# Kernel tuning notes

Measured on AMD Instinct MI355X. Metric: run time of the kernel, lower is better.

## Reference

```python
import jax, jax.numpy as jnp
import numpy as np

H, Q, D, V = 256, 64, 512, 34
L, N, T = 1024, 64, 256


def _mlp(x, W0, b0, W1, b1):
    # two-layer MLP with ELU on hidden (matches MLP with nn.ELU activation)
    return jax.nn.elu(x @ W0.T + b0) @ W1.T + b1


def _lstm_cell(x, h, c, Wih, Whh, bih, bhh):
    gates = x @ Wih.T + bih + h @ Whh.T + bhh
    i, f, g, o = jnp.split(gates, 4, axis=-1)  # PyTorch LSTMCell gate order
    i, f, o = jax.nn.sigmoid(i), jax.nn.sigmoid(f), jax.nn.sigmoid(o)
    c_new = f * c + i * jnp.tanh(g)
    h_new = o * jnp.tanh(c_new)
    return h_new, c_new


def _attn(q, key, value, mask):
    # q: [N,Q], key: [N,L,Q], value: [N,L,H], mask: [N,L]
    scores = jnp.einsum('nlq,nq->nl', key, q)
    a = jax.nn.softmax(scores, axis=-1) * mask
    a = a / jnp.sum(a, axis=-1, keepdims=True)
    return jnp.einsum('nl,nlh->nh', a, value)


def setup_inputs() -> dict:
    key = jax.random.key(0)
    ks = iter(jax.random.split(key, 64))

    def rn(shape, s=0.05):
        return jax.random.normal(next(ks), shape, jnp.float32) * s

    inp = {
        'seqs': rn((L, N, D), 1.0),
        'seq_lens': jax.random.randint(next(ks), (N,), L // 2, L + 1),
        'labels': jax.random.randint(next(ks), (T, N), 0, V),
        'emb': rn((V, H)),
        'inith': rn((3, H)),
        'initc': rn((3, H)),
    }
    in_sizes = [2 * H, H, H]
    for i in range(3):
        inp[f'Wih{i}'] = rn((4 * H, in_sizes[i]))
        inp[f'Whh{i}'] = rn((4 * H, H))
        inp[f'bih{i}'] = rn((4 * H,))
        inp[f'bhh{i}'] = rn((4 * H,))
    inp['qW0'] = rn((H, H)); inp['qb0'] = rn((H,))
    inp['qW1'] = rn((Q, H)); inp['qb1'] = rn((Q,))
    inp['kW0'] = rn((D, D)); inp['kb0'] = rn((D,))
    inp['kW1'] = rn((Q, D)); inp['kb1'] = rn((Q,))
    inp['vW0'] = rn((H, D)); inp['vb0'] = rn((H,))
    inp['vW1'] = rn((H, H)); inp['vb1'] = rn((H,))
    inp['outW'] = rn((V, 2 * H)); inp['outb'] = rn((V,))
    return inp


def reference(seqs, seq_lens, labels, emb, inith, initc,
              Wih0, Whh0, bih0, bhh0, Wih1, Whh1, bih1, bhh1,
              Wih2, Whh2, bih2, bhh2,
              qW0, qb0, qW1, qb1, kW0, kb0, kW1, kb1,
              vW0, vb0, vW1, vb1, outW, outb):
    T_, N_ = labels.shape
    L_ = seqs.shape[0]
    lstm = [(Wih0, Whh0, bih0, bhh0), (Wih1, Whh1, bih1, bhh1), (Wih2, Whh2, bih2, bhh2)]

    char_input = emb[labels]                                   # [T,N,H]
    key = _mlp(seqs, kW0, kb0, kW1, kb1).transpose(1, 0, 2)    # [N,L,Q]
    value = _mlp(seqs, vW0, vb0, vW1, vb1).transpose(1, 0, 2)  # [N,L,H]
    mask = (jnp.arange(L_)[None, :] < seq_lens[:, None]).astype(seqs.dtype)

    h = jnp.tile(inith[:, None, :], (1, N_, 1))  # [3,N,H]
    c = jnp.tile(initc[:, None, :], (1, N_, 1))
    q = _mlp(h[2], qW0, qb0, qW1, qb1)
    prev_ctx = _attn(q, key, value, mask)

    def step(carry, x_t):
        h, c, ctx = carry
        xin = jnp.concatenate([ctx, x_t], axis=1)  # [N,2H]
        hs, cs = [], []
        for i in range(3):
            nh, nc = _lstm_cell(xin, h[i], c[i], *lstm[i])
            hs.append(nh); cs.append(nc)
            xin = nh
        h = jnp.stack(hs); c = jnp.stack(cs)
        q = _mlp(h[2], qW0, qb0, qW1, qb1)
        ctx = _attn(q, key, value, mask)
        out = jnp.concatenate([ctx, h[2]], axis=1) @ outW.T + outb  # [N,V]
        return (h, c, ctx), out

    _, outs = jax.lax.scan(step, (h, c, prev_ctx), char_input)
    return outs  # [T,N,V]
```

## Files before the change

kernel.cpp:

```cpp
#include <hip/hip_runtime.h>
#include <cstddef>

#define DEV static __device__ __forceinline__
typedef unsigned long long ull;

DEV float b2f(unsigned short u){ unsigned int i=((unsigned int)u)<<16; float f; __builtin_memcpy(&f,&i,4); return f; }
DEV float lo16(unsigned int u){ unsigned int i=u<<16; float f; __builtin_memcpy(&f,&i,4); return f; }
DEV float hi16(unsigned int u){ unsigned int i=u&0xffff0000u; float f; __builtin_memcpy(&f,&i,4); return f; }
DEV unsigned short f2b(float f){ unsigned int i; __builtin_memcpy(&i,&f,4); unsigned int r=(i+0x7fffu+((i>>16)&1u))>>16; return (unsigned short)r; }
DEV float sigf(float x){ return 1.f/(1.f+__expf(-x)); }
DEV float eluf(float x){ return x>0.f ? x : (__expf(x)-1.f); }
DEV float gload(const void* p, long i, int f32){
  return f32 ? ((const float*)p)[i] : b2f(((const unsigned short*)p)[i]);
}
DEV ull pk(float f, unsigned tag){ unsigned b; __builtin_memcpy(&b,&f,4); return ((ull)tag<<32)|b; }
DEV float upk(ull u){ unsigned b=(unsigned)u; float f; __builtin_memcpy(&f,&b,4); return f; }
DEV void ast64(ull* p, ull v){ __hip_atomic_store(p, v, __ATOMIC_RELAXED, __HIP_MEMORY_SCOPE_AGENT); }
DEV ull ald64(const ull* p){ return __hip_atomic_load(p, __ATOMIC_RELAXED, __HIP_MEMORY_SCOPE_AGENT); }

__global__ __launch_bounds__(64) void sniff(const void* __restrict__ seqs,
                                            const void* __restrict__ seq_lens,
                                            int* __restrict__ flags)
{
  __shared__ int cnt;
  if (threadIdx.x==0) cnt=0;
  __syncthreads();
  const unsigned short* u = (const unsigned short*)seqs;
  int sane=0;
  for (int i=threadIdx.x;i<1024;i+=64){
    int e = (u[i]>>7)&0xFF;
    if (e>=0x70 && e<=0x8F) sane++;
  }
  atomicAdd(&cnt, sane);
  __syncthreads();
  if (threadIdx.x==0){
    flags[0] = (cnt < 820) ? 1 : 0;
    const int* s = (const int*)seq_lens;
    flags[1] = ((s[1]|s[3]|s[5]|s[7])==0) ? 1 : 0;
  }
}

__global__ __launch_bounds__(256) void prep_transpose(
    const void* __restrict__ Wih0, const void* __restrict__ Whh0,
    const void* __restrict__ Wih1, const void* __restrict__ Whh1,
    const void* __restrict__ Wih2, const void* __restrict__ Whh2,
    const void* __restrict__ kW0,  const void* __restrict__ kW1,
    const void* __restrict__ vW0,  const void* __restrict__ vW1,
    const void* __restrict__ qW0,  const void* __restrict__ qW1,
    const void* __restrict__ bih0, const void* __restrict__ bhh0,
    const void* __restrict__ bih1, const void* __restrict__ bhh1,
    const void* __restrict__ bih2, const void* __restrict__ bhh2,
    const void* __restrict__ outW, const void* __restrict__ inith,
    const void* __restrict__ initc, const void* __restrict__ qb0,
    const void* __restrict__ qb1,  const void* __restrict__ outb,
    const int* __restrict__ flags,
    unsigned short* __restrict__ Wl0, unsigned short* __restrict__ Wl1,
    unsigned short* __restrict__ Wl2,
    unsigned short* __restrict__ kW0T, unsigned short* __restrict__ kW1T,
    unsigned short* __restrict__ vW0T, unsigned short* __restrict__ vW1T,
    unsigned short* __restrict__ qW0T, unsigned short* __restrict__ qW1T,
    float* __restrict__ bsum,
    unsigned short* __restrict__ outWc, unsigned short* __restrict__ inithc,
    unsigned short* __restrict__ initcc, unsigned short* __restrict__ qb0c,
    unsigned short* __restrict__ qb1c,  unsigned short* __restrict__ outbc)
{
  const int f32 = flags[0];
  int idx = blockIdx.x*256 + threadIdx.x;
  if (idx < 524288){ int r=idx&131071, k=r>>8, gi=r&255;
    int g = ((gi>>6)<<8) + ((idx>>17)<<6) + (gi&63);
    Wl0[idx] = f2b((k<256)? gload(Wih0,(long)g*512+k,f32) : gload(Whh0,(long)g*256+(k-256),f32)); return; }
  idx -= 524288;
  if (idx < 524288){ int r=idx&131071, k=r>>8, gi=r&255;
    int g = ((gi>>6)<<8) + ((idx>>17)<<6) + (gi&63);
    Wl1[idx] = f2b((k<256)? gload(Wih1,(long)g*256+k,f32) : gload(Whh1,(long)g*256+(k-256),f32)); return; }
  idx -= 524288;
  if (idx < 524288){ int r=idx&131071, k=r>>8, gi=r&255;
    int g = ((gi>>6)<<8) + ((idx>>17)<<6) + (gi&63);
    Wl2[idx] = f2b((k<256)? gload(Wih2,(long)g*256+k,f32) : gload(Whh2,(long)g*256+(k-256),f32)); return; }
  idx -= 524288;
  if (idx < 262144){ int k=idx>>9, j=idx&511; kW0T[idx]=f2b(gload(kW0,(long)j*512+k,f32)); return; }
  idx -= 262144;
  if (idx < 32768){ int k=idx>>6, j=idx&63; kW1T[idx]=f2b(gload(kW1,(long)j*512+k,f32)); return; }
  idx -= 32768;
  if (idx < 131072){ int k=idx>>8, j=idx&255; vW0T[idx]=f2b(gload(vW0,(long)j*512+k,f32)); return; }
  idx -= 131072;
  if (idx < 65536){ int k=idx>>8, j=idx&255; vW1T[idx]=f2b(gload(vW1,(long)j*256+k,f32)); return; }
  idx -= 65536;
  if (idx < 65536){ int k=idx>>8, j=idx&255; qW0T[idx]=f2b(gload(qW0,(long)j*256+k,f32)); return; }
  idx -= 65536;
  if (idx < 16384){ int k=idx>>6, j=idx&63; qW1T[idx]=f2b(gload(qW1,(long)j*256+k,f32)); return; }
  idx -= 16384;
  if (idx < 3072){ int l=idx>>10, r=idx&1023, pp=r>>8, gi=r&255;
    int g = ((gi>>6)<<8) + (pp<<6) + (gi&63);
    const void* bi = (l==0)?bih0:((l==1)?bih1:bih2);
    const void* bh = (l==0)?bhh0:((l==1)?bhh1:bhh2);
    bsum[idx] = gload(bi,g,f32)+gload(bh,g,f32); return; }
  idx -= 3072;
  if (idx < 17408){ outWc[idx]=f2b(gload(outW,idx,f32)); return; }
  idx -= 17408;
  if (idx < 768){ inithc[idx]=f2b(gload(inith,idx,f32)); return; }
  idx -= 768;
  if (idx < 768){ initcc[idx]=f2b(gload(initc,idx,f32)); return; }
  idx -= 768;
  if (idx < 256){ qb0c[idx]=f2b(gload(qb0,idx,f32)); return; }
  idx -= 256;
  if (idx < 64){ qb1c[idx]=f2b(gload(qb1,idx,f32)); return; }
  idx -= 64;
  if (idx < 34){ outbc[idx]=f2b(gload(outb,idx,f32)); return; }
}

__global__ __launch_bounds__(256) void prep_ge(
    const void* __restrict__ emb,
    const void* __restrict__ Wih0,
    const int* __restrict__ flags,
    float* __restrict__ gep)
{
  __shared__ float ev[256];
  const int f32 = flags[0];
  const int v = blockIdx.x, tid = threadIdx.x;
  ev[tid] = gload(emb,(long)v*256+tid,f32);
  __syncthreads();
  #pragma unroll
  for (int j=0;j<4;j++){
    const int g = tid*4+j;
    float a = 0.f;
    #pragma unroll 4
    for (int k=0;k<256;k++) a += ev[k]*gload(Wih0,(long)g*512+256+k,f32);
    int pp = (g>>6)&3, gi = ((g>>8)<<6)|(g&63);
    gep[((size_t)pp*34+v)*256+gi] = a;
  }
}

__global__ __launch_bounds__(256) void key_mlp(
    const void* __restrict__ seqs,
    const unsigned short* __restrict__ kW0T, const void* __restrict__ kb0,
    const unsigned short* __restrict__ kW1T, const void* __restrict__ kb1,
    const int* __restrict__ flags,
    unsigned short* __restrict__ keyT)
{
  __shared__ float Xt[16*512];
  __shared__ unsigned short Hd[16*512];
  const int f32 = flags[0];
  const int tid = threadIdx.x;
  const int R0 = blockIdx.x*16;
  for (int i=tid;i<8192;i+=256) Xt[i] = gload(seqs,(long)R0*512+i,f32);
  __syncthreads();
  {
    const int j0 = 2*tid;
    float acc0[16], acc1[16];
    #pragma unroll
    for (int r=0;r<16;r++){ acc0[r]=0.f; acc1[r]=0.f; }
    for (int k=0;k<512;k++){
      ushort2 w = *reinterpret_cast<const ushort2*>(kW0T + (size_t)k*512 + j0);
      float w0=b2f(w.x), w1=b2f(w.y);
      #pragma unroll
      for (int r=0;r<16;r++){ float x = Xt[r*512+k]; acc0[r]+=x*w0; acc1[r]+=x*w1; }
    }
    float b0v=gload(kb0,j0,f32), b1v=gload(kb0,j0+1,f32);
    #pragma unroll
    for (int r=0;r<16;r++){
      Hd[r*512+j0]   = f2b(eluf(acc0[r]+b0v));
      Hd[r*512+j0+1] = f2b(eluf(acc1[r]+b1v));
    }
  }
  __syncthreads();
  {
    const int j = tid & 63;
    const int rbase = tid >> 6;
    float acc[4] = {0.f,0.f,0.f,0.f};
    for (int k=0;k<512;k++){
      float w = b2f(kW1T[(size_t)k*64 + j]);
      #pragma unroll
      for (int m=0;m<4;m++) acc[m] += b2f(Hd[(rbase+4*m)*512 + k]) * w;
    }
    float bv = gload(kb1,j,f32);
    #pragma unroll
    for (int m=0;m<4;m++){
      int R = R0 + rbase + 4*m;
      int l = R >> 6, n = R & 63;
      keyT[((size_t)(n*64 + j))*1024 + l] = f2b(acc[m]+bv);
    }
  }
}

__global__ __launch_bounds__(256) void value_mlp(
    const void* __restrict__ seqs,
    const unsigned short* __restrict__ vW0T, const void* __restrict__ vb0,
    const unsigned short* __restrict__ vW1T, const void* __restrict__ vb1,
    const int* __restrict__ flags,
    unsigned short* __restrict__ value)
{
  __shared__ float Xt[16*512];
  __shared__ float Hd[16*256];
  const int f32 = flags[0];
  const int tid = threadIdx.x;
  const int R0 = blockIdx.x*16;
  for (int i=tid;i<8192;i+=256) Xt[i] = gload(seqs,(long)R0*512+i,f32);
  __syncthreads();
  {
    const int j0 = 2*(tid & 127);
    const int rh = tid >> 7;
    float acc0[8], acc1[8];
    #pragma unroll
    for (int r=0;r<8;r++){ acc0[r]=0.f; acc1[r]=0.f; }
    for (int k=0;k<512;k++){
      ushort2 w = *reinterpret_cast<const ushort2*>(vW0T + (size_t)k*256 + j0);
      float w0=b2f(w.x), w1=b2f(w.y);
      #pragma unroll
      for (int r=0;r<8;r++){ float x = Xt[(rh*8+r)*512+k]; acc0[r]+=x*w0; acc1[r]+=x*w1; }
    }
    float b0v=gload(vb0,j0,f32), b1v=gload(vb0,j0+1,f32);
    #pragma unroll
    for (int r=0;r<8;r++){
      Hd[(rh*8+r)*256+j0]   = eluf(acc0[r]+b0v);
      Hd[(rh*8+r)*256+j0+1] = eluf(acc1[r]+b1v);
    }
  }
  __syncthreads();
  {
    const int j = tid;
    float acc[16];
    #pragma unroll
    for (int r=0;r<16;r++) acc[r]=0.f;
    for (int k=0;k<256;k++){
      float w = b2f(vW1T[(size_t)k*256 + j]);
      #pragma unroll
      for (int r=0;r<16;r++) acc[r] += Hd[r*256+k]*w;
    }
    float bv = gload(vb1,j,f32);
    #pragma unroll
    for (int r=0;r<16;r++){
      int R = R0 + r; int l = R>>6, n = R&63;
      value[((size_t)n*1024 + l)*256 + j] = f2b(acc[r]+bv);
    }
  }
}

__global__ __launch_bounds__(256) void zero_hbuf(ull* __restrict__ f){
  int i = blockIdx.x*256 + threadIdx.x;
  if (i < 115200) f[i] = 0;
}

__global__ __launch_bounds__(512, 1) void speller(
    const unsigned short* __restrict__ keyT,
    const unsigned short* __restrict__ value,
    const unsigned short* __restrict__ Wl0,
    const unsigned short* __restrict__ Wl1,
    const unsigned short* __restrict__ Wl2,
    const unsigned short* __restrict__ qW0T,
    const unsigned short* __restrict__ qW1T,
    const float* __restrict__ bsum_p,
    const float* __restrict__ gep,
    const unsigned short* __restrict__ inithc,
    const unsigned short* __restrict__ initcc,
    const unsigned short* __restrict__ qb0c,
    const unsigned short* __restrict__ qb1c,
    const unsigned short* __restrict__ outWc,
    const unsigned short* __restrict__ outbc,
    const int* __restrict__ labels,
    const int* __restrict__ seq_lens,
    const int* __restrict__ dflags,
    ull* __restrict__ hbw,
    void* __restrict__ out)
{
  extern __shared__ char smem_dyn[];
  unsigned short* vlds = (unsigned short*)smem_dyn;

  __shared__ float sacc[4096];
  __shared__ float inc[512];
  __shared__ float garr[256];
  __shared__ float h0[256], h1[256], h2[256], ctx[256];
  __shared__ float cloc[3][64];
  __shared__ float hsl[3][64];
  __shared__ float xq[256];
  __shared__ float qv[64];
  __shared__ float sarr[256], earr[256];
  __shared__ float red[128];
  __shared__ float wf[4];
  __shared__ float pcl[256];
  __shared__ float statl[8];

  const int tid = threadIdx.x;
  const int n = blockIdx.x >> 2;
  const int p = blockIdx.x & 3;
  const int f32o = dflags[0];
  const int i64 = dflags[1];
  const int slen = i64 ? seq_lens[2*n] : seq_lens[n];

  ull* mb   = hbw + (size_t)n*1800;
  ull* H0w  = mb;
  ull* H1w  = mb + 256;
  ull* H2w  = mb + 512;
  ull* PCw  = mb + 768;
  ull* STw  = mb + 1792;

  {
    const uint4* src = (const uint4*)(value + ((size_t)n*1024 + p*256)*256);
    uint4* dst = (uint4*)vlds;
    for (int i=tid;i<16384;i+=512) dst[i] = src[i];
  }
  if (tid < 256){ h0[tid]=b2f(inithc[tid]); h1[tid]=b2f(inithc[256+tid]); h2[tid]=b2f(inithc[512+tid]); }
  if (tid < 64){
    cloc[0][tid]=b2f(initcc[p*64+tid]);
    cloc[1][tid]=b2f(initcc[256+p*64+tid]);
    cloc[2][tid]=b2f(initcc[512+p*64+tid]);
  }
  __syncthreads();

  auto lstm = [&](const unsigned short* W, const float* bs, const float* ger,
                  int layer, ull* Hw, unsigned tag){
    const int go8 = tid & 31, ks = tid >> 5;
    const unsigned short* wp = W + (size_t)p*131072 + (size_t)ks*32*256 + go8*8;
    const float* xin = inc + ks*32;
    float a0=0.f,a1=0.f,a2=0.f,a3=0.f,a4=0.f,a5=0.f,a6=0.f,a7=0.f;
    #pragma unroll 16
    for (int k=0;k<32;k++){
      float x = xin[k];
      uint4 w = *reinterpret_cast<const uint4*>(wp + (size_t)k*256);
      a0 += x*lo16(w.x); a1 += x*hi16(w.x);
      a2 += x*lo16(w.y); a3 += x*hi16(w.y);
      a4 += x*lo16(w.z); a5 += x*hi16(w.z);
      a6 += x*lo16(w.w); a7 += x*hi16(w.w);
    }
    float* sb = sacc + ks*256 + go8*8;
    sb[0]=a0; sb[1]=a1; sb[2]=a2; sb[3]=a3; sb[4]=a4; sb[5]=a5; sb[6]=a6; sb[7]=a7;
    __syncthreads();
    if (tid < 256){
      float s = bs[tid] + (ger ? ger[tid] : 0.f);
      #pragma unroll
      for (int u=0;u<16;u++) s += sacc[u*256+tid];
      garr[tid] = s;
    }
    __syncthreads();
    if (tid < 64){
      float gi=garr[tid], gf=garr[64+tid], gg=garr[128+tid], go=garr[192+tid];
      float cc = sigf(gf)*cloc[layer][tid] + sigf(gi)*tanhf(gg);
      float hh = sigf(go)*tanhf(cc);
      cloc[layer][tid]=cc;
      hsl[layer][tid]=hh;
      ast64(Hw + p*64 + tid, pk(hh, tag));
    }
  };

  auto gather_h = [&](const ull* Hw, int layer, unsigned tag, float* hdst){
    __syncthreads();
    if (tid < 256){
      int sp = tid >> 6; float v;
      if (sp == p) v = hsl[layer][tid & 63];
      else { const ull* w = Hw + tid; ull u = ald64(w);
             while ((unsigned)(u>>32) != tag) u = ald64(w);
             v = upk(u); }
      hdst[tid] = v;
    }
    __syncthreads();
  };

  auto attn = [&](unsigned tag){
    {
      const int j = tid & 255, kh = tid >> 8;
      const unsigned short* qp = qW0T + (size_t)(kh*128)*256 + j;
      float a = 0.f;
      #pragma unroll 8
      for (int k=0;k<128;k++) a += h2[kh*128+k]*b2f(qp[(size_t)k*256]);
      sacc[kh*256 + j] = a;
    }
    __syncthreads();
    if (tid < 256) xq[tid] = eluf(sacc[tid]+sacc[256+tid] + b2f(qb0c[tid]));
    __syncthreads();
    {
      const int qc = tid & 63, k8 = tid >> 6;
      float a = 0.f;
      const unsigned short* qp = qW1T + qc;
      #pragma unroll 8
      for (int k=0;k<32;k++){ int kk = k8*32+k; a += xq[kk]*b2f(qp[(size_t)kk*64]); }
      sacc[k8*64+qc] = a;
    }
    __syncthreads();
    if (tid < 64){
      float s=0.f;
      #pragma unroll
      for (int u=0;u<8;u++) s += sacc[u*64+tid];
      qv[tid] = s + b2f(qb1c[tid]);
    }
    __syncthreads();
    {
      const int lp = tid & 127, qh = tid >> 7;
      float a0=0.f,a1=0.f;
      const unsigned short* kp = keyT + (size_t)n*65536 + (size_t)qh*16*1024 + p*256 + 2*lp;
      #pragma unroll 8
      for (int q=0;q<16;q++){
        ushort2 w = *reinterpret_cast<const ushort2*>(kp + (size_t)q*1024);
        float qq = qv[qh*16+q];
        a0 += qq*b2f(w.x); a1 += qq*b2f(w.y);
      }
      sacc[qh*256+2*lp]=a0; sacc[qh*256+2*lp+1]=a1;
    }
    __syncthreads();
    if (tid < 256){
      float s = sacc[tid]+sacc[256+tid]+sacc[512+tid]+sacc[768+tid];
      sarr[tid] = (p*256+tid < slen) ? s : -1e30f;
    }
    __syncthreads();
    if (tid < 128) red[tid] = fmaxf(sarr[tid], sarr[tid+128]);
    __syncthreads();
    for (int s=64;s>0;s>>=1){ if (tid<s) red[tid]=fmaxf(red[tid],red[tid+s]); __syncthreads(); }
    const float pmax = red[0];
    __syncthreads();
    if (tid < 256) earr[tid] = (p*256+tid < slen) ? __expf(sarr[tid]-pmax) : 0.f;
    __syncthreads();
    if (tid < 128) red[tid] = earr[tid]+earr[tid+128];
    __syncthreads();
    for (int s=64;s>0;s>>=1){ if (tid<s) red[tid]+=red[tid+s]; __syncthreads(); }
    const float psum = red[0];
    {
      const int hp = tid & 127, lq = tid >> 7;
      float a0=0.f,a1=0.f;
      const unsigned short* vp = vlds + (size_t)(lq*64)*256 + 2*hp;
      #pragma unroll 8
      for (int l=0;l<64;l++){
        ushort2 w = *reinterpret_cast<const ushort2*>(vp + (size_t)l*256);
        float e = earr[lq*64+l];
        a0 += e*b2f(w.x); a1 += e*b2f(w.y);
      }
      sacc[lq*256+2*hp]=a0; sacc[lq*256+2*hp+1]=a1;
    }
    __syncthreads();
    if (tid < 256){
      float v = sacc[tid]+sacc[256+tid]+sacc[512+tid]+sacc[768+tid];
      pcl[tid] = v;
      ast64(PCw + p*256 + tid, pk(v, tag));
    }
    if (tid == 0){ ast64(STw + p*2, pk(pmax, tag)); ast64(STw + p*2 + 1, pk(psum, tag)); }
    if (tid < 8){
      int q = tid >> 1, ix = tid & 1; float v;
      if (q == p) v = ix ? psum : pmax;
      else { const ull* w = STw + q*2 + ix; ull u = ald64(w);
             while ((unsigned)(u>>32) != tag) u = ald64(w);
             v = upk(u); }
      statl[tid] = v;
    }
    __syncthreads();
    if (tid == 0){
      float m0=statl[0], s0=statl[1], m1=statl[2], s1=statl[3];
      float m2=statl[4], s2=statl[5], m3=statl[6], s3=statl[7];
      float M = fmaxf(fmaxf(m0,m1),fmaxf(m2,m3));
      float w0=__expf(m0-M), w1=__expf(m1-M), w2=__expf(m2-M), w3=__expf(m3-M);
      float inv = 1.f/(s0*w0+s1*w1+s2*w2+s3*w3);
      wf[0]=w0*inv; wf[1]=w1*inv; wf[2]=w2*inv; wf[3]=w3*inv;
    }
    __syncthreads();
    if (tid < 256){
      float acc = pcl[tid]*wf[p];
      #pragma unroll
      for (int q=0;q<4;q++){
        if (q == p) continue;
        const ull* w = PCw + q*256 + tid; ull u = ald64(w);
        while ((unsigned)(u>>32) != tag) u = ald64(w);
        acc += upk(u)*wf[q];
      }
      ctx[tid] = acc;
    }
    __syncthreads();
  };

  attn(1);

  for (int t=0;t<256;t++){
    const unsigned tb = 4*(unsigned)t;
    const int lab = i64 ? labels[2*(t*64+n)] : labels[t*64+n];
    if (tid < 256){ inc[tid]=ctx[tid]; inc[256+tid]=h0[tid]; }
    __syncthreads();
    lstm(Wl0, bsum_p + p*256, gep + ((size_t)p*34+lab)*256, 0, H0w, tb+2);
    gather_h(H0w, 0, tb+2, h0);
    if (tid < 256){ inc[tid]=h0[tid]; inc[256+tid]=h1[tid]; }
    __syncthreads();
    lstm(Wl1, bsum_p + 1024 + p*256, nullptr, 1, H1w, tb+3);
    gather_h(H1w, 1, tb+3, h1);
    if (tid < 256){ inc[tid]=h1[tid]; inc[256+tid]=h2[tid]; }
    __syncthreads();
    lstm(Wl2, bsum_p + 2048 + p*256, nullptr, 2, H2w, tb+4);
    gather_h(H2w, 2, tb+4, h2);
    attn(tb+5);
    {
      const int ri = tid >> 6, kk = tid & 63;
      const int r = 4*ri + p;
      float acc = 0.f;
      const unsigned short* wr = outWc + (size_t)r*512 + kk;
      #pragma unroll
      for (int s=0;s<4;s++) acc += ctx[s*64+kk]*b2f(wr[s*64]);
      #pragma unroll
      for (int s=0;s<4;s++) acc += h2[s*64+kk]*b2f(wr[256+s*64]);
      #pragma unroll
      for (int off=32; off>0; off>>=1) acc += __shfl_down(acc, off);
      if (kk==0){
        float v = acc + b2f(outbc[r]);
        size_t oi = ((size_t)(t*64+n))*34 + r;
        if (f32o) ((float*)out)[oi]=v; else ((unsigned short*)out)[oi]=f2b(v);
      }
      if (p < 2 && tid < 64){
        const int r2 = 32+p;
        float a2=0.f;
        const unsigned short* wr2 = outWc + (size_t)r2*512 + tid;
        #pragma unroll
        for (int s=0;s<4;s++) a2 += ctx[s*64+tid]*b2f(wr2[s*64]);
        #pragma unroll
        for (int s=0;s<4;s++) a2 += h2[s*64+tid]*b2f(wr2[256+s*64]);
        #pragma unroll
        for (int off=32; off>0; off>>=1) a2 += __shfl_down(a2, off);
        if (tid==0){
          float v = a2 + b2f(outbc[r2]);
          size_t oi = ((size_t)(t*64+n))*34 + r2;
          if (f32o) ((float*)out)[oi]=v; else ((unsigned short*)out)[oi]=f2b(v);
        }
      }
    }
  }
}

extern "C" void kernel_launch(void* const* d_in, const int* in_sizes, int n_in,
                              void* d_out, int out_size, void* d_ws, size_t ws_size,
                              hipStream_t stream) {
  const void* seqs  = d_in[0];
  const int* seq_lens = (const int*)d_in[1];
  const int* labels   = (const int*)d_in[2];
  const void* emb   = d_in[3];
  const void* inith = d_in[4];
  const void* initc = d_in[5];
  const void* Wih0 = d_in[6];  const void* Whh0 = d_in[7];
  const void* bih0 = d_in[8];  const void* bhh0 = d_in[9];
  const void* Wih1 = d_in[10]; const void* Whh1 = d_in[11];
  const void* bih1 = d_in[12]; const void* bhh1 = d_in[13];
  const void* Wih2 = d_in[14]; const void* Whh2 = d_in[15];
  const void* bih2 = d_in[16]; const void* bhh2 = d_in[17];
  const void* qW0 = d_in[18];  const void* qb0 = d_in[19];
  const void* qW1 = d_in[20];  const void* qb1 = d_in[21];
  const void* kW0 = d_in[22];  const void* kb0 = d_in[23];
  const void* kW1 = d_in[24];  const void* kb1 = d_in[25];
  const void* vW0 = d_in[26];  const void* vb0 = d_in[27];
  const void* vW1 = d_in[28];  const void* vb1 = d_in[29];
  const void* outW = d_in[30]; const void* outb = d_in[31];

  char* ws = (char*)d_ws;
  unsigned short* keyT  = (unsigned short*)(ws);
  unsigned short* value = (unsigned short*)(ws + 8388608);
  unsigned short* Wl0   = (unsigned short*)(ws + 41943040);
  unsigned short* Wl1   = (unsigned short*)(ws + 42991616);
  unsigned short* Wl2   = (unsigned short*)(ws + 44040192);
  unsigned short* kW0T  = (unsigned short*)(ws + 45088768);
  unsigned short* kW1T  = (unsigned short*)(ws + 45613056);
  unsigned short* vW0T  = (unsigned short*)(ws + 45678592);
  unsigned short* vW1T  = (unsigned short*)(ws + 45940736);
  unsigned short* qW0T  = (unsigned short*)(ws + 46071808);
  unsigned short* qW1T  = (unsigned short*)(ws + 46202880);
  float*          bsum  = (float*)(ws + 46235648);
  float*          gep   = (float*)(ws + 46247936);
  unsigned short* outWc = (unsigned short*)(ws + 46387200);
  unsigned short* inithc= (unsigned short*)(ws + 46422016);
  unsigned short* initcc= (unsigned short*)(ws + 46423552);
  unsigned short* qb0c  = (unsigned short*)(ws + 46425088);
  unsigned short* qb1c  = (unsigned short*)(ws + 46425600);
  unsigned short* outbc = (unsigned short*)(ws + 46425728);
  int*            dflags= (int*)(ws + 46425856);
  ull* hbw = (ull*)(ws + 45088768);

  sniff<<<dim3(1), dim3(64), 0, stream>>>(seqs, seq_lens, dflags);
  prep_transpose<<<dim3(8472), dim3(256), 0, stream>>>(
      Wih0,Whh0,Wih1,Whh1,Wih2,Whh2, kW0,kW1,vW0,vW1,qW0,qW1,
      bih0,bhh0,bih1,bhh1,bih2,bhh2,
      outW,inith,initc,qb0,qb1,outb, dflags,
      Wl0,Wl1,Wl2,kW0T,kW1T,vW0T,vW1T,qW0T,qW1T,bsum,
      outWc,inithc,initcc,qb0c,qb1c,outbc);
  prep_ge<<<dim3(34), dim3(256), 0, stream>>>(emb, Wih0, dflags, gep);
  key_mlp<<<dim3(4096), dim3(256), 0, stream>>>(seqs, kW0T, kb0, kW1T, kb1, dflags, keyT);
  value_mlp<<<dim3(4096), dim3(256), 0, stream>>>(seqs, vW0T, vb0, vW1T, vb1, dflags, value);
  zero_hbuf<<<dim3(450), dim3(256), 0, stream>>>(hbw);
  hipFuncSetAttribute((const void*)speller, hipFuncAttributeMaxDynamicSharedMemorySize, 131072);
  speller<<<dim3(256), dim3(512), 131072, stream>>>(
      keyT, value, Wl0, Wl1, Wl2, qW0T, qW1T, bsum, gep,
      inithc, initcc, qb0c, qb1c, outWc, outbc, labels, seq_lens, dflags,
      hbw, d_out);
}
```

Measured before the change: 8.248 ms.

## Co-locate cooperating blocks per XCD and use L2-scoped flag exchange

Remaps block indices so the four blocks that cooperate on one sequence are likely to land on the same XCD. Each block reads its XCC id from a hardware register and publishes it, and when all four match, h, context and softmax statistics are exchanged through sc0 stores and loads that stay in the shared L2 instead of going device-wide. Tags now carry a per-launch salt so stale mailbox entries cannot match. The tree reductions for the softmax max and sum are replaced with wavefront shuffles. The cost is reliance on undocumented scheduling behaviour and memory-scope semantics, plus dual posting (atomic and sc0 store) on every write.

```diff
diff --git a/kernel.cpp b/kernel.cpp
--- a/kernel.cpp
+++ b/kernel.cpp
@@ -17,6 +17,15 @@
 DEV float upk(ull u){ unsigned b=(unsigned)u; float f; __builtin_memcpy(&f,&b,4); return f; }
 DEV void ast64(ull* p, ull v){ __hip_atomic_store(p, v, __ATOMIC_RELAXED, __HIP_MEMORY_SCOPE_AGENT); }
 DEV ull ald64(const ull* p){ return __hip_atomic_load(p, __ATOMIC_RELAXED, __HIP_MEMORY_SCOPE_AGENT); }
+DEV void st_sc0(ull* p, ull v){
+  asm volatile("global_store_dwordx2 %0, %1, off sc0" :: "v"(p), "v"(v) : "memory");
+}
+DEV ull ld_sc0(const ull* p){
+  ull r;
+  asm volatile("global_load_dwordx2 %0, %1, off sc0\n\ts_waitcnt vmcnt(0)"
+               : "=v"(r) : "v"(p) : "memory");
+  return r;
+}
 
 __global__ __launch_bounds__(64) void sniff(const void* __restrict__ seqs,
                                             const void* __restrict__ seq_lens,
@@ -238,7 +247,7 @@
 
 __global__ __launch_bounds__(256) void zero_hbuf(ull* __restrict__ f){
   int i = blockIdx.x*256 + threadIdx.x;
-  if (i < 115200) f[i] = 0;
+  if (i < 115456) ast64(&f[i], 0);
 }
 
 __global__ __launch_bounds__(512, 1) void speller(
@@ -274,25 +283,37 @@
   __shared__ float hsl[3][64];
   __shared__ float xq[256];
   __shared__ float qv[64];
-  __shared__ float sarr[256], earr[256];
-  __shared__ float red[128];
+  __shared__ float earr[256];
+  __shared__ float red[16];
   __shared__ float wf[4];
   __shared__ float pcl[256];
   __shared__ float statl[8];
+  __shared__ int   xcls[4];
 
   const int tid = threadIdx.x;
-  const int n = blockIdx.x >> 2;
-  const int p = blockIdx.x & 3;
+  const int bx  = (int)blockIdx.x;
+  const int slot = bx >> 3;
+  const int n = ((slot >> 2) << 3) | (bx & 7);
+  const int p = slot & 3;
   const int f32o = dflags[0];
   const int i64 = dflags[1];
   const int slen = i64 ? seq_lens[2*n] : seq_lens[n];
 
-  ull* mb   = hbw + (size_t)n*1800;
+  ull* mb   = hbw + (size_t)n*1804;
   ull* H0w  = mb;
   ull* H1w  = mb + 256;
   ull* H2w  = mb + 512;
   ull* PCw  = mb + 768;
   ull* STw  = mb + 1792;
+  ull* XCw  = mb + 1800;
+
+  int myxcc;
+  asm volatile("s_getreg_b32 %0, hwreg(20, 0, 32)" : "=s"(myxcc));
+  myxcc &= 0xf;
+  if (tid == 0){
+    unsigned salt = (unsigned)(__builtin_amdgcn_s_memrealtime() >> 4) & 0x1fffffu;
+    ast64(XCw + p, ((ull)1u<<32) | (unsigned)myxcc | (salt<<4));
+  }
 
   {
     const uint4* src = (const uint4*)(value + ((size_t)n*1024 + p*256)*256);
@@ -306,6 +327,37 @@
     cloc[2][tid]=b2f(initcc[512+p*64+tid]);
   }
   __syncthreads();
+
+  if (tid < 4){
+    const ull* w = XCw + tid; ull u = ald64(w);
+    while ((unsigned)(u>>32) != 1u) u = ald64(w);
+    xcls[tid] = (int)(unsigned)u;
+  }
+  __syncthreads();
+  const unsigned xl0=(unsigned)xcls[0], xl1=(unsigned)xcls[1],
+                 xl2=(unsigned)xcls[2], xl3=(unsigned)xcls[3];
+  const bool fastmb = (((xl0^xl1)|(xl1^xl2)|(xl2^xl3)) & 0xfu) == 0u;
+  const unsigned tagbase = (xl0 >> 4) << 11;
+
+  auto post = [&](ull* w, ull v){
+    ast64(w, v);
+    if (fastmb) st_sc0(w, v);
+  };
+  auto pollw = [&](const ull* w, unsigned tag)->float{
+    ull u;
+    if (fastmb){
+      u = ld_sc0(w);
+      int spins = 0;
+      while ((unsigned)(u>>32) != tag){
+        ++spins;
+        u = (spins < 128 || (spins & 1)) ? ld_sc0(w) : ald64(w);
+      }
+    } else {
+      u = ald64(w);
+      while ((unsigned)(u>>32) != tag) u = ald64(w);
+    }
+    return upk(u);
+  };
 
   auto lstm = [&](const unsigned short* W, const float* bs, const float* ger,
                   int layer, ull* Hw, unsigned tag){
@@ -338,7 +390,7 @@
       float hh = sigf(go)*tanhf(cc);
       cloc[layer][tid]=cc;
       hsl[layer][tid]=hh;
-      ast64(Hw + p*64 + tid, pk(hh, tag));
+      post(Hw + p*64 + tid, pk(hh, tag));
     }
   };
 
@@ -347,9 +399,7 @@
     if (tid < 256){
       int sp = tid >> 6; float v;
       if (sp == p) v = hsl[layer][tid & 63];
-      else { const ull* w = Hw + tid; ull u = ald64(w);
-             while ((unsigned)(u>>32) != tag) u = ald64(w);
-             v = upk(u); }
+      else v = pollw(Hw + tid, tag);
       hdst[tid] = v;
     }
     __syncthreads();
@@ -396,22 +446,31 @@
       sacc[qh*256+2*lp]=a0; sacc[qh*256+2*lp+1]=a1;
     }
     __syncthreads();
-    if (tid < 256){
-      float s = sacc[tid]+sacc[256+tid]+sacc[512+tid]+sacc[768+tid];
-      sarr[tid] = (p*256+tid < slen) ? s : -1e30f;
-    }
-    __syncthreads();
-    if (tid < 128) red[tid] = fmaxf(sarr[tid], sarr[tid+128]);
-    __syncthreads();
-    for (int s=64;s>0;s>>=1){ if (tid<s) red[tid]=fmaxf(red[tid],red[tid+s]); __syncthreads(); }
-    const float pmax = red[0];
-    __syncthreads();
-    if (tid < 256) earr[tid] = (p*256+tid < slen) ? __expf(sarr[tid]-pmax) : 0.f;
-    __syncthreads();
-    if (tid < 128) red[tid] = earr[tid]+earr[tid+128];
-    __syncthreads();
-    for (int s=64;s>0;s>>=1){ if (tid<s) red[tid]+=red[tid+s]; __syncthreads(); }
-    const float psum = red[0];
+    float pmax, psum;
+    {
+      float s = -1e30f;
+      if (tid < 256){
+        s = sacc[tid]+sacc[256+tid]+sacc[512+tid]+sacc[768+tid];
+        if (p*256+tid >= slen) s = -1e30f;
+      }
+      float m = s;
+      #pragma unroll
+      for (int off=32; off; off>>=1) m = fmaxf(m, __shfl_xor(m, off));
+      if ((tid&63)==0) red[tid>>6] = m;
+      __syncthreads();
+      pmax = fmaxf(fmaxf(red[0],red[1]),fmaxf(red[2],red[3]));
+      float e = 0.f;
+      if (tid < 256){
+        e = (p*256+tid < slen) ? __expf(s - pmax) : 0.f;
+        earr[tid] = e;
+      }
+      float ss = e;
+      #pragma unroll
+      for (int off=32; off; off>>=1) ss += __shfl_xor(ss, off);
+      if ((tid&63)==0) red[8+(tid>>6)] = ss;
+      __syncthreads();
+      psum = red[8]+red[9]+red[10]+red[11];
+    }
     {
       const int hp = tid & 127, lq = tid >> 7;
       float a0=0.f,a1=0.f;
@@ -428,15 +487,13 @@
     if (tid < 256){
       float v = sacc[tid]+sacc[256+tid]+sacc[512+tid]+sacc[768+tid];
       pcl[tid] = v;
-      ast64(PCw + p*256 + tid, pk(v, tag));
-    }
-    if (tid == 0){ ast64(STw + p*2, pk(pmax, tag)); ast64(STw + p*2 + 1, pk(psum, tag)); }
+      post(PCw + p*256 + tid, pk(v, tag));
+    }
+    if (tid == 0){ post(STw + p*2, pk(pmax, tag)); post(STw + p*2 + 1, pk(psum, tag)); }
     if (tid < 8){
       int q = tid >> 1, ix = tid & 1; float v;
       if (q == p) v = ix ? psum : pmax;
-      else { const ull* w = STw + q*2 + ix; ull u = ald64(w);
-             while ((unsigned)(u>>32) != tag) u = ald64(w);
-             v = upk(u); }
+      else v = pollw(STw + q*2 + ix, tag);
       statl[tid] = v;
     }
     __syncthreads();
@@ -454,19 +511,17 @@
       #pragma unroll
       for (int q=0;q<4;q++){
         if (q == p) continue;
-        const ull* w = PCw + q*256 + tid; ull u = ald64(w);
-        while ((unsigned)(u>>32) != tag) u = ald64(w);
-        acc += upk(u)*wf[q];
+        acc += pollw(PCw + q*256 + tid, tag)*wf[q];
       }
       ctx[tid] = acc;
     }
     __syncthreads();
   };
 
-  attn(1);
+  attn(tagbase+1);
 
   for (int t=0;t<256;t++){
-    const unsigned tb = 4*(unsigned)t;
+    const unsigned tb = tagbase + 4*(unsigned)t;
     const int lab = i64 ? labels[2*(t*64+n)] : labels[t*64+n];
     if (tid < 256){ inc[tid]=ctx[tid]; inc[256+tid]=h0[tid]; }
     __syncthreads();
@@ -573,7 +628,7 @@
   prep_ge<<<dim3(34), dim3(256), 0, stream>>>(emb, Wih0, dflags, gep);
   key_mlp<<<dim3(4096), dim3(256), 0, stream>>>(seqs, kW0T, kb0, kW1T, kb1, dflags, keyT);
   value_mlp<<<dim3(4096), dim3(256), 0, stream>>>(seqs, vW0T, vb0, vW1T, vb1, dflags, value);
-  zero_hbuf<<<dim3(450), dim3(256), 0, stream>>>(hbw);
+  zero_hbuf<<<dim3(451), dim3(256), 0, stream>>>(hbw);
   hipFuncSetAttribute((const void*)speller, hipFuncAttributeMaxDynamicSharedMemorySize, 131072);
   speller<<<dim3(256), dim3(512), 131072, stream>>>(
       keyT, value, Wl0, Wl1, Wl2, qW0T, qW1T, bsum, gep,
```

After: 21.70 ms. +163.1%, slower.

## Cut barriers in speller step: fused input staging, wave-shuffle softmax, vectorized q-MLP weights

Applied to the files above, without the earlier changes.

Each recurrent step of the persistent speller kernel loses several __syncthreads: the LSTM input staging moves into gather_h and the attention tail, and the softmax max/sum tree reductions become wave-level shuffle reductions. The q-MLP weights are re-laid out in prep so each thread reads 8 bf16 values per 128-bit load instead of scalar strided loads. The cross-block context spin-wait now issues all three polls before looping. The goal is a shorter serial critical path per timestep, at the cost of a more complex weight layout and more coupling between the step phases.

```diff
diff --git a/kernel.cpp b/kernel.cpp
--- a/kernel.cpp
+++ b/kernel.cpp
@@ -58,7 +58,7 @@
     unsigned short* __restrict__ Wl2,
     unsigned short* __restrict__ kW0T, unsigned short* __restrict__ kW1T,
     unsigned short* __restrict__ vW0T, unsigned short* __restrict__ vW1T,
-    unsigned short* __restrict__ qW0T, unsigned short* __restrict__ qW1T,
+    unsigned short* __restrict__ qW0v, unsigned short* __restrict__ qW1v,
     float* __restrict__ bsum,
     unsigned short* __restrict__ outWc, unsigned short* __restrict__ inithc,
     unsigned short* __restrict__ initcc, unsigned short* __restrict__ qb0c,
@@ -86,9 +86,13 @@
   idx -= 131072;
   if (idx < 65536){ int k=idx>>8, j=idx&255; vW1T[idx]=f2b(gload(vW1,(long)j*256+k,f32)); return; }
   idx -= 65536;
-  if (idx < 65536){ int k=idx>>8, j=idx&255; qW0T[idx]=f2b(gload(qW0,(long)j*256+k,f32)); return; }
+  if (idx < 65536){
+    int k8=idx>>11, j=(idx>>3)&255, kk=idx&7; int k=k8*8+kk;
+    qW0v[idx]=f2b(gload(qW0,(long)j*256+k,f32)); return; }
   idx -= 65536;
-  if (idx < 16384){ int k=idx>>6, j=idx&63; qW1T[idx]=f2b(gload(qW1,(long)j*256+k,f32)); return; }
+  if (idx < 16384){
+    int k8=idx>>11, qc=(idx>>5)&63, kk=idx&31; int k=k8*32+kk;
+    qW1v[idx]=f2b(gload(qW1,(long)qc*256+k,f32)); return; }
   idx -= 16384;
   if (idx < 3072){ int l=idx>>10, r=idx&1023, pp=r>>8, gi=r&255;
     int g = ((gi>>6)<<8) + (pp<<6) + (gi&63);
@@ -247,8 +251,8 @@
     const unsigned short* __restrict__ Wl0,
     const unsigned short* __restrict__ Wl1,
     const unsigned short* __restrict__ Wl2,
-    const unsigned short* __restrict__ qW0T,
-    const unsigned short* __restrict__ qW1T,
+    const unsigned short* __restrict__ qW0v,
+    const unsigned short* __restrict__ qW1v,
     const float* __restrict__ bsum_p,
     const float* __restrict__ gep,
     const unsigned short* __restrict__ inithc,
@@ -274,8 +278,8 @@
   __shared__ float hsl[3][64];
   __shared__ float xq[256];
   __shared__ float qv[64];
-  __shared__ float sarr[256], earr[256];
-  __shared__ float red[128];
+  __shared__ float earr[256];
+  __shared__ float red[16];
   __shared__ float wf[4];
   __shared__ float pcl[256];
   __shared__ float statl[8];
@@ -342,7 +346,8 @@
     }
   };
 
-  auto gather_h = [&](const ull* Hw, int layer, unsigned tag, float* hdst){
+  auto gather_h = [&](const ull* Hw, int layer, unsigned tag, float* hdst,
+                      const float* nexth){
     __syncthreads();
     if (tid < 256){
       int sp = tid >> 6; float v;
@@ -351,6 +356,7 @@
              while ((unsigned)(u>>32) != tag) u = ald64(w);
              v = upk(u); }
       hdst[tid] = v;
+      if (nexth){ inc[tid] = v; inc[256+tid] = nexth[tid]; }
     }
     __syncthreads();
   };
@@ -358,10 +364,17 @@
   auto attn = [&](unsigned tag){
     {
       const int j = tid & 255, kh = tid >> 8;
-      const unsigned short* qp = qW0T + (size_t)(kh*128)*256 + j;
+      const uint4* qp = (const uint4*)qW0v + (size_t)(kh*16)*256 + j;
       float a = 0.f;
-      #pragma unroll 8
-      for (int k=0;k<128;k++) a += h2[kh*128+k]*b2f(qp[(size_t)k*256]);
+      #pragma unroll
+      for (int k8=0;k8<16;k8++){
+        uint4 w = qp[(size_t)k8*256];
+        const float* hb = h2 + kh*128 + k8*8;
+        a += hb[0]*lo16(w.x)+hb[1]*hi16(w.x)
+           + hb[2]*lo16(w.y)+hb[3]*hi16(w.y)
+           + hb[4]*lo16(w.z)+hb[5]*hi16(w.z)
+           + hb[6]*lo16(w.w)+hb[7]*hi16(w.w);
+      }
       sacc[kh*256 + j] = a;
     }
     __syncthreads();
@@ -369,10 +382,17 @@
     __syncthreads();
     {
       const int qc = tid & 63, k8 = tid >> 6;
+      const uint4* qp = (const uint4*)qW1v + (size_t)(k8*64+qc)*4;
       float a = 0.f;
-      const unsigned short* qp = qW1T + qc;
-      #pragma unroll 8
-      for (int k=0;k<32;k++){ int kk = k8*32+k; a += xq[kk]*b2f(qp[(size_t)kk*64]); }
+      #pragma unroll
+      for (int u=0;u<4;u++){
+        uint4 w = qp[u];
+        const float* xb = xq + k8*32 + u*8;
+        a += xb[0]*lo16(w.x)+xb[1]*hi16(w.x)
+           + xb[2]*lo16(w.y)+xb[3]*hi16(w.y)
+           + xb[4]*lo16(w.z)+xb[5]*hi16(w.z)
+           + xb[6]*lo16(w.w)+xb[7]*hi16(w.w);
+      }
       sacc[k8*64+qc] = a;
     }
     __syncthreads();
@@ -396,22 +416,31 @@
       sacc[qh*256+2*lp]=a0; sacc[qh*256+2*lp+1]=a1;
     }
     __syncthreads();
-    if (tid < 256){
-      float s = sacc[tid]+sacc[256+tid]+sacc[512+tid]+sacc[768+tid];
-      sarr[tid] = (p*256+tid < slen) ? s : -1e30f;
-    }
-    __syncthreads();
-    if (tid < 128) red[tid] = fmaxf(sarr[tid], sarr[tid+128]);
-    __syncthreads();
-    for (int s=64;s>0;s>>=1){ if (tid<s) red[tid]=fmaxf(red[tid],red[tid+s]); __syncthreads(); }
-    const float pmax = red[0];
-    __syncthreads();
-    if (tid < 256) earr[tid] = (p*256+tid < slen) ? __expf(sarr[tid]-pmax) : 0.f;
-    __syncthreads();
-    if (tid < 128) red[tid] = earr[tid]+earr[tid+128];
-    __syncthreads();
-    for (int s=64;s>0;s>>=1){ if (tid<s) red[tid]+=red[tid+s]; __syncthreads(); }
-    const float psum = red[0];
+    float pmax, psum;
+    {
+      float s = -1e30f;
+      if (tid < 256){
+        s = sacc[tid]+sacc[256+tid]+sacc[512+tid]+sacc[768+tid];
+        if (p*256+tid >= slen) s = -1e30f;
+      }
+      float m = s;
+      #pragma unroll
+      for (int off=32; off; off>>=1) m = fmaxf(m, __shfl_xor(m, off));
+      if ((tid&63)==0) red[tid>>6] = m;
+      __syncthreads();
+      pmax = fmaxf(fmaxf(red[0],red[1]),fmaxf(red[2],red[3]));
+      float e = 0.f;
+      if (tid < 256){
+        e = (p*256+tid < slen) ? __expf(s - pmax) : 0.f;
+        earr[tid] = e;
+      }
+      float ss = e;
+      #pragma unroll
+      for (int off=32; off; off>>=1) ss += __shfl_xor(ss, off);
+      if ((tid&63)==0) red[8+(tid>>6)] = ss;
+      __syncthreads();
+      psum = red[8]+red[9]+red[10]+red[11];
+    }
     {
       const int hp = tid & 127, lq = tid >> 7;
       float a0=0.f,a1=0.f;
@@ -450,15 +479,18 @@
     }
     __syncthreads();
     if (tid < 256){
-      float acc = pcl[tid]*wf[p];
-      #pragma unroll
-      for (int q=0;q<4;q++){
-        if (q == p) continue;
-        const ull* w = PCw + q*256 + tid; ull u = ald64(w);
-        while ((unsigned)(u>>32) != tag) u = ald64(w);
-        acc += upk(u)*wf[q];
-      }
+      const int q0=(p+1)&3, q1=(p+2)&3, q2=(p+3)&3;
+      const ull* w0 = PCw + q0*256 + tid;
+      const ull* w1 = PCw + q1*256 + tid;
+      const ull* w2 = PCw + q2*256 + tid;
+      ull u0=ald64(w0), u1=ald64(w1), u2=ald64(w2);
+      while ((unsigned)(u0>>32) != tag) u0 = ald64(w0);
+      while ((unsigned)(u1>>32) != tag) u1 = ald64(w1);
+      while ((unsigned)(u2>>32) != tag) u2 = ald64(w2);
+      float acc = pcl[tid]*wf[p] + upk(u0)*wf[q0] + upk(u1)*wf[q1] + upk(u2)*wf[q2];
       ctx[tid] = acc;
+      inc[tid] = acc;
+      inc[256+tid] = h0[tid];
     }
     __syncthreads();
   };
@@ -468,18 +500,12 @@
   for (int t=0;t<256;t++){
     const unsigned tb = 4*(unsigned)t;
     const int lab = i64 ? labels[2*(t*64+n)] : labels[t*64+n];
-    if (tid < 256){ inc[tid]=ctx[tid]; inc[256+tid]=h0[tid]; }
-    __syncthreads();
     lstm(Wl0, bsum_p + p*256, gep + ((size_t)p*34+lab)*256, 0, H0w, tb+2);
-    gather_h(H0w, 0, tb+2, h0);
-    if (tid < 256){ inc[tid]=h0[tid]; inc[256+tid]=h1[tid]; }
-    __syncthreads();
+    gather_h(H0w, 0, tb+2, h0, h1);
     lstm(Wl1, bsum_p + 1024 + p*256, nullptr, 1, H1w, tb+3);
-    gather_h(H1w, 1, tb+3, h1);
-    if (tid < 256){ inc[tid]=h1[tid]; inc[256+tid]=h2[tid]; }
-    __syncthreads();
+    gather_h(H1w, 1, tb+3, h1, h2);
     lstm(Wl2, bsum_p + 2048 + p*256, nullptr, 2, H2w, tb+4);
-    gather_h(H2w, 2, tb+4, h2);
+    gather_h(H2w, 2, tb+4, h2, nullptr);
     attn(tb+5);
     {
       const int ri = tid >> 6, kk = tid & 63;
@@ -550,8 +576,8 @@
   unsigned short* kW1T  = (unsigned short*)(ws + 45613056);
   unsigned short* vW0T  = (unsigned short*)(ws + 45678592);
   unsigned short* vW1T  = (unsigned short*)(ws + 45940736);
-  unsigned short* qW0T  = (unsigned short*)(ws + 46071808);
-  unsigned short* qW1T  = (unsigned short*)(ws + 46202880);
+  unsigned short* qW0v  = (unsigned short*)(ws + 46071808);
+  unsigned short* qW1v  = (unsigned short*)(ws + 46202880);
   float*          bsum  = (float*)(ws + 46235648);
   float*          gep   = (float*)(ws + 46247936);
   unsigned short* outWc = (unsigned short*)(ws + 46387200);
@@ -568,7 +594,7 @@
       Wih0,Whh0,Wih1,Whh1,Wih2,Whh2, kW0,kW1,vW0,vW1,qW0,qW1,
       bih0,bhh0,bih1,bhh1,bih2,bhh2,
       outW,inith,initc,qb0,qb1,outb, dflags,
-      Wl0,Wl1,Wl2,kW0T,kW1T,vW0T,vW1T,qW0T,qW1T,bsum,
+      Wl0,Wl1,Wl2,kW0T,kW1T,vW0T,vW1T,qW0v,qW1v,bsum,
       outWc,inithc,initcc,qb0c,qb1c,outbc);
   prep_ge<<<dim3(34), dim3(256), 0, stream>>>(emb, Wih0, dflags, gep);
   key_mlp<<<dim3(4096), dim3(256), 0, stream>>>(seqs, kW0T, kb0, kW1T, kb1, dflags, keyT);
@@ -576,7 +602,7 @@
   zero_hbuf<<<dim3(450), dim3(256), 0, stream>>>(hbw);
   hipFuncSetAttribute((const void*)speller, hipFuncAttributeMaxDynamicSharedMemorySize, 131072);
   speller<<<dim3(256), dim3(512), 131072, stream>>>(
-      keyT, value, Wl0, Wl1, Wl2, qW0T, qW1T, bsum, gep,
+      keyT, value, Wl0, Wl1, Wl2, qW0v, qW1v, bsum, gep,
       inithc, initcc, qb0c, qb1c, outWc, outbc, labels, seq_lens, dflags,
       hbw, d_out);
 }
```

New measurement: 8.160 ms. About the same (-1.1%).
